# Kernel tuning notes

Measured on AMD Instinct MI355X. Metric: run time of the kernel, lower is better.

The kernel has to match this reference:

```python
import jax, jax.numpy as jnp
import numpy as np

B, T, C, H, D = 131072, 8, 32, 4, 8  # batch, context_window, n_embed, num_heads, head_size


def setup_inputs() -> dict:
    key = jax.random.key(0)
    ks = jax.random.split(key, 7)
    s = 0.02
    return {
        "x": jax.random.normal(ks[0], (B, T, C), dtype=jnp.float32),
        "Wq": jax.random.normal(ks[1], (H, C, D), dtype=jnp.float32) * s,
        "Wk": jax.random.normal(ks[2], (H, C, D), dtype=jnp.float32) * s,
        "Wv": jax.random.normal(ks[3], (H, C, D), dtype=jnp.float32) * s,
        "Wf": jax.random.normal(ks[4], (C, C), dtype=jnp.float32) * s,
        "bf": jax.random.normal(ks[5], (C,), dtype=jnp.float32) * s,
    }


def reference(x, Wq, Wk, Wv, Wf, bf):
    # Multi-head causal self-attention (heads batched instead of Python loop)
    q = jnp.einsum('btc,hcd->bhtd', x, Wq)
    k = jnp.einsum('btc,hcd->bhtd', x, Wk)
    v = jnp.einsum('btc,hcd->bhtd', x, Wv)
    scale = jnp.asarray(D, x.dtype) ** -0.5
    scores = jnp.einsum('bhtd,bhsd->bhts', q, k) * scale  # (B,H,T,T)
    causal = jnp.tril(jnp.ones((T, T), dtype=bool))
    scores = jnp.where(causal, scores, jnp.asarray(-jnp.inf, scores.dtype))
    wei = jax.nn.softmax(scores, axis=-1)
    out = jnp.einsum('bhts,bhsd->bhtd', wei, v)
    out = out.transpose(0, 2, 1, 3).reshape(out.shape[0], T, C)  # concat heads
    # FeedForward: Linear + ReLU (note: no residuals in this Block)
    return jax.nn.relu(out @ Wf + bf)
```

## Files before the change

### kernel.cpp

```cpp
#include <hip/hip_runtime.h>
#include <stdint.h>

#define B_ 131072
#define T_ 8
#define C_ 32
#define H_ 4
#define D_ 8

typedef __attribute__((ext_vector_type(8))) short bf16x8;
typedef __attribute__((ext_vector_type(4))) float f32x4;

union FragU { bf16x8 v; uint32_t u[4]; };

__device__ inline uint32_t cvt_pk_bf16(float lo, float hi) {
    uint32_t r;
    asm("v_cvt_pk_bf16_f32 %0, %1, %2" : "=v"(r) : "v"(lo), "v"(hi));
    return r;
}

#define QKV_STRIDE 100
#define TILES_PER_WAVE 4

__global__ __launch_bounds__(256, 6) void attn_block_mfma(
    const float* __restrict__ X,
    const float* __restrict__ Wq,
    const float* __restrict__ Wk,
    const float* __restrict__ Wv,
    const float* __restrict__ Wf,
    const float* __restrict__ bfb,
    float* __restrict__ Y)
{
    __shared__ float lds[4][QKV_STRIDE * 16];
    const int wid  = threadIdx.x >> 6;
    const int lane = threadIdx.x & 63;
    const int cc = lane & 15;
    const int gg = lane >> 4;
    float* qkv = &lds[wid][0];

    const float scale = 0.35355339059327373f;

    FragU bW[6];
    {
        const float* const Ws[3] = { Wq, Wk, Wv };
        #pragma unroll
        for (int tau = 0; tau < 6; ++tau) {
            const float* Wm = Ws[tau >> 1];
            const int col = (tau & 1) * 16 + cc;
            const int head = col >> 3, d = col & 7;
            float f[8];
            #pragma unroll
            for (int jj = 0; jj < 8; ++jj)
                f[jj] = Wm[head * 256 + (gg * 8 + jj) * 8 + d];
            if (tau < 2) {
                #pragma unroll
                for (int jj = 0; jj < 8; ++jj) f[jj] *= scale;
            }
            bW[tau].u[0] = cvt_pk_bf16(f[0], f[1]);
            bW[tau].u[1] = cvt_pk_bf16(f[2], f[3]);
            bW[tau].u[2] = cvt_pk_bf16(f[4], f[5]);
            bW[tau].u[3] = cvt_pk_bf16(f[6], f[7]);
        }
    }
    FragU bF[2];
    {
        #pragma unroll
        for (int tau = 0; tau < 2; ++tau) {
            const int col = tau * 16 + cc;
            float f[8];
            #pragma unroll
            for (int jj = 0; jj < 8; ++jj)
                f[jj] = Wf[(gg * 8 + jj) * 32 + col];
            bF[tau].u[0] = cvt_pk_bf16(f[0], f[1]);
            bF[tau].u[1] = cvt_pk_bf16(f[2], f[3]);
            bF[tau].u[2] = cvt_pk_bf16(f[4], f[5]);
            bF[tau].u[3] = cvt_pk_bf16(f[6], f[7]);
        }
    }
    const float bias0 = bfb[cc];
    const float bias1 = bfb[cc + 16];

    const int waveGlobal = blockIdx.x * 4 + wid;
    const f32x4 z = { 0.f, 0.f, 0.f, 0.f };

    int rowbase = waveGlobal * (16 * TILES_PER_WAVE);
    const float* xp = X + (size_t)(rowbase + cc) * 32 + gg * 8;
    float4 xa = *(const float4*)xp;
    float4 xb = *(const float4*)(xp + 4);

    #pragma unroll 1
    for (int it = 0; it < TILES_PER_WAVE; ++it) {
        rowbase = waveGlobal * (16 * TILES_PER_WAVE) + it * 16;

        FragU aX;
        aX.u[0] = cvt_pk_bf16(xa.x, xa.y);
        aX.u[1] = cvt_pk_bf16(xa.z, xa.w);
        aX.u[2] = cvt_pk_bf16(xb.x, xb.y);
        aX.u[3] = cvt_pk_bf16(xb.z, xb.w);

        {
            const int itn = (it + 1 < TILES_PER_WAVE) ? it + 1 : it;
            const float* xpn = X + (size_t)(waveGlobal * (16 * TILES_PER_WAVE) + itn * 16 + cc) * 32 + gg * 8;
            xa = *(const float4*)xpn;
            xb = *(const float4*)(xpn + 4);
        }

        f32x4 cq[6];
        #pragma unroll
        for (int tau = 0; tau < 6; ++tau)
            cq[tau] = __builtin_amdgcn_mfma_f32_16x16x32_bf16(aX.v, bW[tau].v, z, 0, 0, 0);

        #pragma unroll
        for (int tau = 0; tau < 6; ++tau) {
            #pragma unroll
            for (int r = 0; r < 4; ++r)
                qkv[(gg * 4 + r) * QKV_STRIDE + tau * 16 + cc] = cq[tau][r];
        }

        const int tpos = cc & 7, bb = cc >> 3;

        const float* qr = qkv + cc * QKV_STRIDE + gg * 8;
        const float4 qa = *(const float4*)qr;
        const float4 qb = *(const float4*)(qr + 4);

        float sc[8];
        #pragma unroll
        for (int s = 0; s < 8; ++s) {
            const float* kr = qkv + (bb * 8 + s) * QKV_STRIDE + 32 + gg * 8;
            const float4 ka = *(const float4*)kr;
            const float4 kb = *(const float4*)(kr + 4);
            float dot =          qa.x * ka.x;
            dot = fmaf(qa.y, ka.y, dot);
            dot = fmaf(qa.z, ka.z, dot);
            dot = fmaf(qa.w, ka.w, dot);
            dot = fmaf(qb.x, kb.x, dot);
            dot = fmaf(qb.y, kb.y, dot);
            dot = fmaf(qb.z, kb.z, dot);
            dot = fmaf(qb.w, kb.w, dot);
            sc[s] = (s <= tpos) ? dot : -1.0e30f;
        }
        float m = sc[0];
        #pragma unroll
        for (int s = 1; s < 8; ++s) m = fmaxf(m, sc[s]);
        float e[8], sum = 0.f;
        #pragma unroll
        for (int s = 0; s < 8; ++s) { e[s] = __expf(sc[s] - m); sum += e[s]; }
        const float winv = 1.0f / sum;

        float4 o03 = { 0.f, 0.f, 0.f, 0.f }, o47 = { 0.f, 0.f, 0.f, 0.f };
        #pragma unroll
        for (int s = 0; s < 8; ++s) {
            const float* vr = qkv + (bb * 8 + s) * QKV_STRIDE + 64 + gg * 8;
            const float4 va = *(const float4*)vr;
            const float4 vb = *(const float4*)(vr + 4);
            o03.x = fmaf(e[s], va.x, o03.x);
            o03.y = fmaf(e[s], va.y, o03.y);
            o03.z = fmaf(e[s], va.z, o03.z);
            o03.w = fmaf(e[s], va.w, o03.w);
            o47.x = fmaf(e[s], vb.x, o47.x);
            o47.y = fmaf(e[s], vb.y, o47.y);
            o47.z = fmaf(e[s], vb.z, o47.z);
            o47.w = fmaf(e[s], vb.w, o47.w);
        }

        FragU aO;
        aO.u[0] = cvt_pk_bf16(o03.x * winv, o03.y * winv);
        aO.u[1] = cvt_pk_bf16(o03.z * winv, o03.w * winv);
        aO.u[2] = cvt_pk_bf16(o47.x * winv, o47.y * winv);
        aO.u[3] = cvt_pk_bf16(o47.z * winv, o47.w * winv);

        const f32x4 y0 = __builtin_amdgcn_mfma_f32_16x16x32_bf16(aO.v, bF[0].v, z, 0, 0, 0);
        const f32x4 y1 = __builtin_amdgcn_mfma_f32_16x16x32_bf16(aO.v, bF[1].v, z, 0, 0, 0);

        #pragma unroll
        for (int r = 0; r < 4; ++r) {
            float* yp = Y + (size_t)(rowbase + gg * 4 + r) * 32;
            yp[cc]      = fmaxf(y0[r] + bias0, 0.f);
            yp[cc + 16] = fmaxf(y1[r] + bias1, 0.f);
        }
    }
}

extern "C" void kernel_launch(void* const* d_in, const int* in_sizes, int n_in,
                              void* d_out, int out_size, void* d_ws, size_t ws_size,
                              hipStream_t stream)
{
    const float* X  = (const float*)d_in[0];
    const float* Wq = (const float*)d_in[1];
    const float* Wk = (const float*)d_in[2];
    const float* Wv = (const float*)d_in[3];
    const float* Wf = (const float*)d_in[4];
    const float* bf = (const float*)d_in[5];
    float* Y = (float*)d_out;

    const int rows = B_ * T_;
    const int rows_per_block = 4 * TILES_PER_WAVE * 16;
    dim3 grid(rows / rows_per_block), block(256);
    hipLaunchKernelGGL(attn_block_mfma, grid, block, 0, stream,
                       X, Wq, Wk, Wv, Wf, bf, Y);
}
```

Baseline: 56.28 us.

## Switch to fp16 MFMA with transposed fp16 QKV staging in LDS

Replaces bf16 MFMA with fp16 MFMA and computes QKV transposed (weights as A operand), so each lane packs its four outputs into fp16 and writes one 8-byte LDS store instead of four scalar fp32 stores. Q/K/V are read back as 16-byte fp16 vectors, which halves LDS traffic. The log2(e) factor is folded into the Q scale so softmax can use exp2f, and the weighted V sum is accumulated with packed fp16 math. The intent is to cut LDS instruction count and ALU work, at the cost of reduced accumulation precision in fp16 and possible fp16 overflow or round-to-zero error.

```diff
diff --git a/kernel.cpp b/kernel.cpp
--- a/kernel.cpp
+++ b/kernel.cpp
@@ -7,19 +7,18 @@
 #define H_ 4
 #define D_ 8
 
-typedef __attribute__((ext_vector_type(8))) short bf16x8;
-typedef __attribute__((ext_vector_type(4))) float f32x4;
+#define TILES_PER_WAVE 4
+#define ROWB 208
 
-union FragU { bf16x8 v; uint32_t u[4]; };
+typedef __fp16   fp16x2 __attribute__((ext_vector_type(2)));
+typedef _Float16 f16x8 __attribute__((ext_vector_type(8)));
+typedef float    f32x4 __attribute__((ext_vector_type(4)));
 
-__device__ inline uint32_t cvt_pk_bf16(float lo, float hi) {
-    uint32_t r;
-    asm("v_cvt_pk_bf16_f32 %0, %1, %2" : "=v"(r) : "v"(lo), "v"(hi));
-    return r;
+union H2U { fp16x2 h; uint32_t u; };
+
+__device__ inline uint32_t pk(float lo, float hi) {
+    H2U t; t.h = __builtin_amdgcn_cvt_pkrtz(lo, hi); return t.u;
 }
-
-#define QKV_STRIDE 100
-#define TILES_PER_WAVE 4
 
 __global__ __launch_bounds__(256, 6) void attn_block_mfma(
     const float* __restrict__ X,
@@ -30,50 +29,43 @@
     const float* __restrict__ bfb,
     float* __restrict__ Y)
 {
-    __shared__ float lds[4][QKV_STRIDE * 16];
+    __shared__ __align__(16) char ldsraw[4][16 * ROWB];
     const int wid  = threadIdx.x >> 6;
     const int lane = threadIdx.x & 63;
     const int cc = lane & 15;
     const int gg = lane >> 4;
-    float* qkv = &lds[wid][0];
+    char* qkv = &ldsraw[wid][0];
 
-    const float scale = 0.35355339059327373f;
+    const float qscale = 0.35355339059327373f * 1.4426950408889634f;
 
-    FragU bW[6];
+    f16x8 aW[6];
     {
         const float* const Ws[3] = { Wq, Wk, Wv };
         #pragma unroll
         for (int tau = 0; tau < 6; ++tau) {
             const float* Wm = Ws[tau >> 1];
-            const int col = (tau & 1) * 16 + cc;
-            const int head = col >> 3, d = col & 7;
-            float f[8];
+            const int f = (tau & 1) * 16 + cc;
+            const int head = f >> 3, d = f & 7;
+            float fv[8];
             #pragma unroll
-            for (int jj = 0; jj < 8; ++jj)
-                f[jj] = Wm[head * 256 + (gg * 8 + jj) * 8 + d];
+            for (int j = 0; j < 8; ++j)
+                fv[j] = Wm[head * (C_ * D_) + (gg * 8 + j) * D_ + d];
             if (tau < 2) {
                 #pragma unroll
-                for (int jj = 0; jj < 8; ++jj) f[jj] *= scale;
+                for (int j = 0; j < 8; ++j) fv[j] *= qscale;
             }
-            bW[tau].u[0] = cvt_pk_bf16(f[0], f[1]);
-            bW[tau].u[1] = cvt_pk_bf16(f[2], f[3]);
-            bW[tau].u[2] = cvt_pk_bf16(f[4], f[5]);
-            bW[tau].u[3] = cvt_pk_bf16(f[6], f[7]);
+            #pragma unroll
+            for (int j = 0; j < 8; ++j) aW[tau][j] = (_Float16)fv[j];
         }
     }
-    FragU bF[2];
+    f16x8 bF[2];
     {
         #pragma unroll
         for (int tau = 0; tau < 2; ++tau) {
             const int col = tau * 16 + cc;
-            float f[8];
             #pragma unroll
-            for (int jj = 0; jj < 8; ++jj)
-                f[jj] = Wf[(gg * 8 + jj) * 32 + col];
-            bF[tau].u[0] = cvt_pk_bf16(f[0], f[1]);
-            bF[tau].u[1] = cvt_pk_bf16(f[2], f[3]);
-            bF[tau].u[2] = cvt_pk_bf16(f[4], f[5]);
-            bF[tau].u[3] = cvt_pk_bf16(f[6], f[7]);
+            for (int j = 0; j < 8; ++j)
+                bF[tau][j] = (_Float16)Wf[(gg * 8 + j) * C_ + col];
         }
     }
     const float bias0 = bfb[cc];
@@ -83,7 +75,7 @@
     const f32x4 z = { 0.f, 0.f, 0.f, 0.f };
 
     int rowbase = waveGlobal * (16 * TILES_PER_WAVE);
-    const float* xp = X + (size_t)(rowbase + cc) * 32 + gg * 8;
+    const float* xp = X + (size_t)(rowbase + cc) * C_ + gg * 8;
     float4 xa = *(const float4*)xp;
     float4 xb = *(const float4*)(xp + 4);
 
@@ -91,89 +83,67 @@
     for (int it = 0; it < TILES_PER_WAVE; ++it) {
         rowbase = waveGlobal * (16 * TILES_PER_WAVE) + it * 16;
 
-        FragU aX;
-        aX.u[0] = cvt_pk_bf16(xa.x, xa.y);
-        aX.u[1] = cvt_pk_bf16(xa.z, xa.w);
-        aX.u[2] = cvt_pk_bf16(xb.x, xb.y);
-        aX.u[3] = cvt_pk_bf16(xb.z, xb.w);
+        f16x8 aX;
+        aX[0] = (_Float16)xa.x; aX[1] = (_Float16)xa.y;
+        aX[2] = (_Float16)xa.z; aX[3] = (_Float16)xa.w;
+        aX[4] = (_Float16)xb.x; aX[5] = (_Float16)xb.y;
+        aX[6] = (_Float16)xb.z; aX[7] = (_Float16)xb.w;
 
         {
             const int itn = (it + 1 < TILES_PER_WAVE) ? it + 1 : it;
-            const float* xpn = X + (size_t)(waveGlobal * (16 * TILES_PER_WAVE) + itn * 16 + cc) * 32 + gg * 8;
+            const float* xpn = X + (size_t)(waveGlobal * (16 * TILES_PER_WAVE) + itn * 16 + cc) * C_ + gg * 8;
             xa = *(const float4*)xpn;
             xb = *(const float4*)(xpn + 4);
         }
 
-        f32x4 cq[6];
-        #pragma unroll
-        for (int tau = 0; tau < 6; ++tau)
-            cq[tau] = __builtin_amdgcn_mfma_f32_16x16x32_bf16(aX.v, bW[tau].v, z, 0, 0, 0);
-
         #pragma unroll
         for (int tau = 0; tau < 6; ++tau) {
-            #pragma unroll
-            for (int r = 0; r < 4; ++r)
-                qkv[(gg * 4 + r) * QKV_STRIDE + tau * 16 + cc] = cq[tau][r];
+            f32x4 cq = __builtin_amdgcn_mfma_f32_16x16x32_f16(aW[tau], aX, z, 0, 0, 0);
+            uint2 w2;
+            w2.x = pk(cq[0], cq[1]);
+            w2.y = pk(cq[2], cq[3]);
+            *(uint2*)(qkv + cc * ROWB + (tau * 16 + gg * 4) * 2) = w2;
         }
 
         const int tpos = cc & 7, bb = cc >> 3;
 
-        const float* qr = qkv + cc * QKV_STRIDE + gg * 8;
-        const float4 qa = *(const float4*)qr;
-        const float4 qb = *(const float4*)(qr + 4);
+        const f16x8 q8 = *(const f16x8*)(qkv + cc * ROWB + gg * 16);
+        float qf[8];
+        #pragma unroll
+        for (int j = 0; j < 8; ++j) qf[j] = (float)q8[j];
 
         float sc[8];
         #pragma unroll
         for (int s = 0; s < 8; ++s) {
-            const float* kr = qkv + (bb * 8 + s) * QKV_STRIDE + 32 + gg * 8;
-            const float4 ka = *(const float4*)kr;
-            const float4 kb = *(const float4*)(kr + 4);
-            float dot =          qa.x * ka.x;
-            dot = fmaf(qa.y, ka.y, dot);
-            dot = fmaf(qa.z, ka.z, dot);
-            dot = fmaf(qa.w, ka.w, dot);
-            dot = fmaf(qb.x, kb.x, dot);
-            dot = fmaf(qb.y, kb.y, dot);
-            dot = fmaf(qb.z, kb.z, dot);
-            dot = fmaf(qb.w, kb.w, dot);
-            sc[s] = (s <= tpos) ? dot : -1.0e30f;
+            const f16x8 k8 = *(const f16x8*)(qkv + (bb * 8 + s) * ROWB + 64 + gg * 16);
+            float acc = 0.f;
+            #pragma unroll
+            for (int j = 0; j < 8; ++j) acc = fmaf(qf[j], (float)k8[j], acc);
+            sc[s] = (s <= tpos) ? acc : -1.0e30f;
         }
         float m = sc[0];
         #pragma unroll
         for (int s = 1; s < 8; ++s) m = fmaxf(m, sc[s]);
         float e[8], sum = 0.f;
         #pragma unroll
-        for (int s = 0; s < 8; ++s) { e[s] = __expf(sc[s] - m); sum += e[s]; }
+        for (int s = 0; s < 8; ++s) { e[s] = exp2f(sc[s] - m); sum += e[s]; }
         const float winv = 1.0f / sum;
 
-        float4 o03 = { 0.f, 0.f, 0.f, 0.f }, o47 = { 0.f, 0.f, 0.f, 0.f };
+        f16x8 o8 = { (_Float16)0, (_Float16)0, (_Float16)0, (_Float16)0,
+                     (_Float16)0, (_Float16)0, (_Float16)0, (_Float16)0 };
         #pragma unroll
         for (int s = 0; s < 8; ++s) {
-            const float* vr = qkv + (bb * 8 + s) * QKV_STRIDE + 64 + gg * 8;
-            const float4 va = *(const float4*)vr;
-            const float4 vb = *(const float4*)(vr + 4);
-            o03.x = fmaf(e[s], va.x, o03.x);
-            o03.y = fmaf(e[s], va.y, o03.y);
-            o03.z = fmaf(e[s], va.z, o03.z);
-            o03.w = fmaf(e[s], va.w, o03.w);
-            o47.x = fmaf(e[s], vb.x, o47.x);
-            o47.y = fmaf(e[s], vb.y, o47.y);
-            o47.z = fmaf(e[s], vb.z, o47.z);
-            o47.w = fmaf(e[s], vb.w, o47.w);
+            const f16x8 v8 = *(const f16x8*)(qkv + (bb * 8 + s) * ROWB + 128 + gg * 16);
+            const _Float16 wsh = (_Float16)(e[s] * winv);
+            o8 += v8 * wsh;
         }
 
-        FragU aO;
-        aO.u[0] = cvt_pk_bf16(o03.x * winv, o03.y * winv);
-        aO.u[1] = cvt_pk_bf16(o03.z * winv, o03.w * winv);
-        aO.u[2] = cvt_pk_bf16(o47.x * winv, o47.y * winv);
-        aO.u[3] = cvt_pk_bf16(o47.z * winv, o47.w * winv);
-
-        const f32x4 y0 = __builtin_amdgcn_mfma_f32_16x16x32_bf16(aO.v, bF[0].v, z, 0, 0, 0);
-        const f32x4 y1 = __builtin_amdgcn_mfma_f32_16x16x32_bf16(aO.v, bF[1].v, z, 0, 0, 0);
+        const f32x4 y0 = __builtin_amdgcn_mfma_f32_16x16x32_f16(o8, bF[0], z, 0, 0, 0);
+        const f32x4 y1 = __builtin_amdgcn_mfma_f32_16x16x32_f16(o8, bF[1], z, 0, 0, 0);
 
         #pragma unroll
         for (int r = 0; r < 4; ++r) {
-            float* yp = Y + (size_t)(rowbase + gg * 4 + r) * 32;
+            float* yp = Y + (size_t)(rowbase + gg * 4 + r) * C_;
             yp[cc]      = fmaxf(y0[r] + bias0, 0.f);
             yp[cc + 16] = fmaxf(y1[r] + bias1, 0.f);
         }
```

New measurement: 91.57 us. 1.63x slower.
